# Kernel optimization log

Measured on AMD Instinct MI355X. Metric: run time of the kernel, lower is better.

The kernel has to match this reference:

```python
import jax, jax.numpy as jnp
import numpy as np

N, E, B = 100000, 640000, 256
F_IN, HID, HEADS = 128, 128, 4
C = HID // HEADS  # 32 channels per head
NEG_SLOPE = 0.2


def _p(key, shape, scale=0.1):
    return (jax.random.normal(key, shape) * scale).astype(jnp.float32)


def setup_inputs() -> dict:
    key = jax.random.key(0)
    ks = jax.random.split(key, 24)
    inp = {
        "x": jax.random.normal(ks[0], (N, F_IN), jnp.float32),
        "edge_index": jax.random.randint(ks[1], (2, E), 0, N),
        "batch": jnp.sort(jax.random.randint(ks[2], (N,), 0, B)),
        "w_in": _p(ks[3], (F_IN, HID)),
        "b_in": jnp.zeros((HID,), jnp.float32),
    }
    for i in range(3):
        inp[f"w{i}"] = _p(ks[4 + 4 * i], (HID, HEADS * C))
        inp[f"asrc{i}"] = _p(ks[5 + 4 * i], (HEADS, C))
        inp[f"adst{i}"] = _p(ks[6 + 4 * i], (HEADS, C))
        inp[f"b{i}"] = jnp.zeros((HID if i < 2 else C,), jnp.float32)
    inp["w_fp"] = _p(ks[20], (C, HID)); inp["b_fp"] = jnp.zeros((HID,), jnp.float32)
    inp["w_m1"] = _p(ks[21], (HID, HID // 2)); inp["b_m1"] = jnp.zeros((HID // 2,), jnp.float32)
    inp["w_m2"] = _p(ks[22], (HID // 2, 1)); inp["b_m2"] = jnp.zeros((1,), jnp.float32)
    return inp


def _gat(x, src, dst, W, a_src, a_dst, bias, concat):
    """PyG-style GATConv (edge_dim=None, eval mode, self-loops pre-appended)."""
    n = x.shape[0]
    H, Ch = a_src.shape
    h = (x @ W).reshape(n, H, Ch)                     # [N,H,C]
    al_s = (h * a_src).sum(-1)                        # [N,H]
    al_d = (h * a_dst).sum(-1)                        # [N,H]
    logit = jax.nn.leaky_relu(al_s[src] + al_d[dst], NEG_SLOPE)  # [Etot,H]
    # segment softmax over incoming edges of each dst node
    m = jax.ops.segment_max(logit, dst, num_segments=n)
    e = jnp.exp(logit - m[dst])
    s = jax.ops.segment_sum(e, dst, num_segments=n)
    alpha = e / (s[dst] + 1e-16)                      # [Etot,H]
    out = jax.ops.segment_sum(h[src] * alpha[:, :, None], dst, num_segments=n)  # [N,H,C]
    out = out.reshape(n, H * Ch) if concat else out.mean(axis=1)
    return out + bias


def reference(x, edge_index, batch, w_in, b_in,
              w0, asrc0, adst0, b0, w1, asrc1, adst1, b1, w2, asrc2, adst2, b2,
              w_fp, b_fp, w_m1, b_m1, w_m2, b_m2):
    n = x.shape[0]
    loops = jnp.arange(n, dtype=edge_index.dtype)
    src = jnp.concatenate([edge_index[0], loops])     # add self loops (PyG default)
    dst = jnp.concatenate([edge_index[1], loops])
    h = x @ w_in + b_in
    h = jax.nn.elu(_gat(h, src, dst, w0, asrc0, adst0, b0, True))
    h = jax.nn.elu(_gat(h, src, dst, w1, asrc1, adst1, b1, True))
    h = jax.nn.elu(_gat(h, src, dst, w2, asrc2, adst2, b2, False))  # [N,C]
    cnt = jax.ops.segment_sum(jnp.ones((n,), h.dtype), batch, num_segments=B)
    pooled = jax.ops.segment_sum(h, batch, num_segments=B) / jnp.maximum(cnt, 1.0)[:, None]
    out = pooled @ w_fp + b_fp                        # final_proj (out dim 32 != 128)
    hm = jax.nn.relu(out @ w_m1 + b_m1)
    return hm @ w_m2 + b_m2                           # [B,1]
```

## Files before the change

### kernel.cpp

```cpp
#include <hip/hip_runtime.h>

#define NEG 0.2f

typedef short s16x8 __attribute__((ext_vector_type(8)));
typedef float f32x4 __attribute__((ext_vector_type(4)));

__device__ __forceinline__ float lrelu(float x) { return x >= 0.f ? x : NEG * x; }
__device__ __forceinline__ float elu1(float x) { return x > 0.f ? x : __expf(x) - 1.f; }

__device__ __forceinline__ unsigned bf16rn(float f) {
    unsigned u = __float_as_uint(f);
    u += 0x7fffu + ((u >> 16) & 1u);
    return u >> 16;
}
__device__ __forceinline__ float bf16tof(ushort h) {
    return __uint_as_float(((unsigned)h) << 16);
}
__device__ __forceinline__ float bf16lo(unsigned u) { return __uint_as_float(u << 16); }
__device__ __forceinline__ float bf16hi(unsigned u) { return __uint_as_float(u & 0xffff0000u); }

__global__ void hist_kernel(const int* __restrict__ dst, int e, int n, int* __restrict__ deg) {
    int p = blockIdx.x & 7;
    int s = blockIdx.x >> 3;
    int nslices = gridDim.x >> 3;
    int rng = (n + 7) >> 3;
    int lo = p * rng, hi = min(n, lo + rng);
    int chunk = (e + nslices - 1) / nslices;
    int i0 = s * chunk, i1 = min(e, i0 + chunk);
    for (int i = i0 + threadIdx.x; i < i1; i += blockDim.x) {
        int d = dst[i];
        if (d >= lo && d < hi) atomicAdd(&deg[d], 1);
    }
}

__device__ __forceinline__ int waveIncScanI(int v, int lane) {
#pragma unroll
    for (int off = 1; off < 64; off <<= 1) {
        int u = __shfl_up(v, off);
        if (lane >= off) v += u;
    }
    return v;
}

__global__ void scan1_kernel(const int* __restrict__ deg, int nk,
                             int* __restrict__ rowp, int* __restrict__ bsums) {
    int t = threadIdx.x;
    int base = blockIdx.x * 2048 + t * 8;
    int vals[8];
    int sum = 0;
#pragma unroll
    for (int i = 0; i < 8; ++i) {
        int idx = base + i;
        int v = (idx < nk) ? deg[idx] : 0;
        vals[i] = sum;
        sum += v;
    }
    int lane = t & 63, w = t >> 6;
    int inc = waveIncScanI(sum, lane);
    __shared__ int wsums[4];
    if (lane == 63) wsums[w] = inc;
    __syncthreads();
    int wpre = 0;
#pragma unroll
    for (int i = 0; i < 3; ++i) wpre += (i < w) ? wsums[i] : 0;
    int exc = wpre + inc - sum;
#pragma unroll
    for (int i = 0; i < 8; ++i) {
        int idx = base + i;
        if (idx < nk) rowp[idx] = exc + vals[i];
    }
    if (t == 255) bsums[blockIdx.x] = wpre + inc;
}

__global__ void scan3_kernel(int* __restrict__ rowp, const int* __restrict__ bsums,
                             int nk, int total, int* __restrict__ cursor) {
    int g = blockIdx.x;
    __shared__ int spre;
    if (threadIdx.x < 64) {
        int lane = threadIdx.x;
        int v = 0;
        for (int base = lane; base < g; base += 64) v += bsums[base];
#pragma unroll
        for (int off = 32; off > 0; off >>= 1) v += __shfl_xor(v, off);
        if (lane == 0) spre = v;
    }
    __syncthreads();
    int pre = spre;
    int base = g * 2048 + threadIdx.x * 8;
#pragma unroll
    for (int i = 0; i < 8; ++i) {
        int idx = base + i;
        if (idx < nk) {
            int v = rowp[idx] + pre;
            rowp[idx] = v;
            cursor[idx] = v;
        } else if (idx == nk) {
            rowp[nk] = total;
        }
    }
}

__global__ void fill_kernel(const int* __restrict__ src, const int* __restrict__ dst, int e,
                            int n, int* __restrict__ cursor, int* __restrict__ col) {
    int p = blockIdx.x & 7;
    int s = blockIdx.x >> 3;
    int nslices = gridDim.x >> 3;
    int rng = (n + 7) >> 3;
    int lo = p * rng, hi = min(n, lo + rng);
    int chunk = (e + nslices - 1) / nslices;
    int i0 = s * chunk, i1 = min(e, i0 + chunk);
    for (int i = i0 + threadIdx.x; i < i1; i += blockDim.x) {
        int d = dst[i];
        if (d >= lo && d < hi) {
            int pos = atomicAdd(&cursor[d], 1);
            col[pos] = src[i];
        }
    }
}

__global__ void wpack_kernel(const float* __restrict__ w0, const float* __restrict__ w1,
                             const float* __restrict__ w2, const float* __restrict__ w3,
                             ushort* __restrict__ whi, ushort* __restrict__ wlo) {
    int idx = blockIdx.x * 256 + threadIdx.x;
    int layer = idx >> 14, e = idx & 16383;
    const float* W = layer == 0 ? w0 : layer == 1 ? w1 : layer == 2 ? w2 : w3;
    int k = e >> 7, c = e & 127;
    float w = W[e];
    ushort hi = (ushort)bf16rn(w);
    ushort lo = (ushort)bf16rn(w - bf16tof(hi));
    int kt = k >> 5, kk = k & 31, j = kk & 7;
    int ln = ((kk >> 3) << 4) | (c & 15);
    int ntg = c >> 4;
    int pos = (layer << 14) + (((kt << 3) + ntg) * 64 + ln) * 8 + j;
    whi[pos] = hi;
    wlo[pos] = lo;
}

template <bool BIAS, bool AL, bool ABF16>
__global__ __launch_bounds__(512, 4) void gemm_mfma_kernel(
    const void* __restrict__ Av, const ushort* __restrict__ whi, const ushort* __restrict__ wlo,
    const float* __restrict__ bias, ushort* __restrict__ outb, int n, int ntiles,
    const float* __restrict__ asrc, const float* __restrict__ adst,
    float* __restrict__ als, float* __restrict__ ald) {
    __shared__ s16x8 ahi[2][4][64];
    __shared__ s16x8 alo[2][4][64];
    int t = threadIdx.x;
    int wid = t >> 6, lane = t & 63;
    int ntp = wid & 3;
    int mhalf = wid >> 2;

    const s16x8* wph = (const s16x8*)whi;
    const s16x8* wpl = (const s16x8*)wlo;
    s16x8 wh[4][2], wl[4][2];
#pragma unroll
    for (int kt = 0; kt < 4; ++kt)
#pragma unroll
        for (int j = 0; j < 2; ++j) {
            int ntg = ntp * 2 + j;
            wh[kt][j] = wph[((kt << 3) + ntg) * 64 + lane];
            wl[kt][j] = wpl[((kt << 3) + ntg) * 64 + lane];
        }

    int c0 = ntp * 32 + (lane & 15);
    int c1 = c0 + 16;
    float bv0 = 0.f, bv1 = 0.f;
    if (BIAS) { bv0 = bias[c0]; bv1 = bias[c1]; }
    float as0 = 0.f, as1 = 0.f, ad0 = 0.f, ad1 = 0.f;
    if (AL) {
        as0 = asrc[ntp * 32 + (lane & 15)];
        as1 = asrc[ntp * 32 + 16 + (lane & 15)];
        ad0 = adst[ntp * 32 + (lane & 15)];
        ad1 = adst[ntp * 32 + 16 + (lane & 15)];
    }

    int srow = t >> 4, skoct = t & 15;
    int smh = srow >> 4, skt = skoct >> 2;
    int sln = ((skoct & 3) << 4) | (srow & 15);

    for (int tile = blockIdx.x; tile < ntiles; tile += gridDim.x) {
        int r0 = tile * 32;
        {
            int gr = r0 + srow;
            if (ABF16) {
                const ushort* Ab = (const ushort*)Av;
                s16x8 hi = {0, 0, 0, 0, 0, 0, 0, 0};
                if (gr < n) hi = *(const s16x8*)(Ab + (size_t)gr * 128 + skoct * 8);
                ahi[smh][skt][sln] = hi;
            } else {
                const float* Af = (const float*)Av;
                float4 v0 = make_float4(0.f, 0.f, 0.f, 0.f), v1 = v0;
                if (gr < n) {
                    const float4* rp = (const float4*)(Af + (size_t)gr * 128 + skoct * 8);
                    v0 = rp[0];
                    v1 = rp[1];
                }
                float f[8] = {v0.x, v0.y, v0.z, v0.w, v1.x, v1.y, v1.z, v1.w};
                s16x8 hi, lo;
#pragma unroll
                for (int j = 0; j < 8; ++j) {
                    ushort h = (ushort)bf16rn(f[j]);
                    hi[j] = (short)h;
                    lo[j] = (short)bf16rn(f[j] - bf16tof(h));
                }
                ahi[smh][skt][sln] = hi;
                alo[smh][skt][sln] = lo;
            }
        }
        __syncthreads();

        f32x4 acc0 = {0.f, 0.f, 0.f, 0.f};
        f32x4 acc1 = {0.f, 0.f, 0.f, 0.f};
#pragma unroll
        for (int kt = 0; kt < 4; ++kt) {
            s16x8 ah = ahi[mhalf][kt][lane];
            if (ABF16) {
                acc0 = __builtin_amdgcn_mfma_f32_16x16x32_bf16(ah, wh[kt][0], acc0, 0, 0, 0);
                acc0 = __builtin_amdgcn_mfma_f32_16x16x32_bf16(ah, wl[kt][0], acc0, 0, 0, 0);
                acc1 = __builtin_amdgcn_mfma_f32_16x16x32_bf16(ah, wh[kt][1], acc1, 0, 0, 0);
                acc1 = __builtin_amdgcn_mfma_f32_16x16x32_bf16(ah, wl[kt][1], acc1, 0, 0, 0);
            } else {
                s16x8 al = alo[mhalf][kt][lane];
                acc0 = __builtin_amdgcn_mfma_f32_16x16x32_bf16(ah, wh[kt][0], acc0, 0, 0, 0);
                acc0 = __builtin_amdgcn_mfma_f32_16x16x32_bf16(ah, wl[kt][0], acc0, 0, 0, 0);
                acc0 = __builtin_amdgcn_mfma_f32_16x16x32_bf16(al, wh[kt][0], acc0, 0, 0, 0);
                acc1 = __builtin_amdgcn_mfma_f32_16x16x32_bf16(ah, wh[kt][1], acc1, 0, 0, 0);
                acc1 = __builtin_amdgcn_mfma_f32_16x16x32_bf16(ah, wl[kt][1], acc1, 0, 0, 0);
                acc1 = __builtin_amdgcn_mfma_f32_16x16x32_bf16(al, wh[kt][1], acc1, 0, 0, 0);
            }
        }

        int rbase = r0 + mhalf * 16 + (lane >> 4) * 4;
#pragma unroll
        for (int i = 0; i < 4; ++i) {
            int r = rbase + i;
            if (r < n) {
                outb[(size_t)r * 128 + c0] = (ushort)bf16rn(acc0[i] + bv0);
                outb[(size_t)r * 128 + c1] = (ushort)bf16rn(acc1[i] + bv1);
            }
        }
        if (AL) {
#pragma unroll
            for (int i = 0; i < 4; ++i) {
                float ps = acc0[i] * as0 + acc1[i] * as1;
                float pd = acc0[i] * ad0 + acc1[i] * ad1;
                ps += __shfl_xor(ps, 1); ps += __shfl_xor(ps, 2);
                ps += __shfl_xor(ps, 4); ps += __shfl_xor(ps, 8);
                pd += __shfl_xor(pd, 1); pd += __shfl_xor(pd, 2);
                pd += __shfl_xor(pd, 4); pd += __shfl_xor(pd, 8);
                int r = rbase + i;
                if ((lane & 15) == 0 && r < n) {
                    als[r * 4 + ntp] = ps;
                    ald[r * 4 + ntp] = pd;
                }
            }
        }
        __syncthreads();
    }
}

template <bool CONCAT>
__global__ void agg_kernel(const ushort* __restrict__ hp, const float* __restrict__ als,
                           const float* __restrict__ ald_, const int* __restrict__ rowp,
                           const int* __restrict__ col, const float* __restrict__ bias,
                           ushort* __restrict__ outb, float* __restrict__ outf, int n) {
    int lane = threadIdx.x & 63;
    int hl = lane & 31;
    int wid = (blockIdx.x * blockDim.x + threadIdx.x) >> 6;
    int d = wid * 2 + (lane >> 5);
    bool valid = d < n;
    int dc = valid ? d : (n - 1);

    int h = hl >> 3;
    int c4 = hl * 4;
    int hh = hl & 3;
    int jl = hl >> 2;
    int bshf = lane & 32;

    int start = rowp[dc];
    int end = valid ? rowp[dc + 1] : start;

    float aldv_hh = ald_[dc * 4 + hh];
    float eself = __expf(lrelu(als[dc * 4 + h] + ald_[dc * 4 + h]));

    uint2 sv = *(const uint2*)(hp + (size_t)dc * 128 + c4);
    float a0 = eself * bf16lo(sv.x), a1 = eself * bf16hi(sv.x);
    float a2 = eself * bf16lo(sv.y), a3 = eself * bf16hi(sv.y);
    float esum = eself;

    int iters = (end - start + 7) >> 3;
    int oiters = __shfl_xor(iters, 32);
    int maxit = iters > oiters ? iters : oiters;
    unsigned nclamp = (unsigned)(n - 1);

    for (int it = 0; it < maxit; ++it) {
        int p0 = start + it * 8;
        bool act = p0 < end;
        int pc = act ? p0 : start;
        int4 ca = *(const int4*)(col + pc);
        int4 cb = *(const int4*)(col + pc + 4);
        unsigned se = (unsigned)col[pc + jl];
        se = se > nclamp ? nclamp : se;
        float ee = __expf(lrelu(als[(size_t)se * 4 + hh] + aldv_hh));
        ee = (act && (p0 + jl < end)) ? ee : 0.f;

#define EDGE(JJ, SRC)                                                              \
        {                                                                          \
            float ej = __shfl(ee, bshf | (JJ << 2) | h);                           \
            unsigned sju = (unsigned)(SRC);                                        \
            sju = sju > nclamp ? nclamp : sju;                                     \
            uint2 uv = *(const uint2*)(hp + (size_t)sju * 128 + c4);               \
            a0 += ej * bf16lo(uv.x); a1 += ej * bf16hi(uv.x);                      \
            a2 += ej * bf16lo(uv.y); a3 += ej * bf16hi(uv.y);                      \
            esum += ej;                                                            \
        }
        EDGE(0, ca.x) EDGE(1, ca.y) EDGE(2, ca.z) EDGE(3, ca.w)
        EDGE(4, cb.x) EDGE(5, cb.y) EDGE(6, cb.z) EDGE(7, cb.w)
#undef EDGE
    }

    float inv = 1.f / (esum + 1e-16f);
    a0 *= inv; a1 *= inv; a2 *= inv; a3 *= inv;
    if (CONCAT) {
        if (valid) {
            float o0 = elu1(a0 + bias[c4]);
            float o1 = elu1(a1 + bias[c4 + 1]);
            float o2 = elu1(a2 + bias[c4 + 2]);
            float o3 = elu1(a3 + bias[c4 + 3]);
            uint2 pk;
            pk.x = bf16rn(o0) | (bf16rn(o1) << 16);
            pk.y = bf16rn(o2) | (bf16rn(o3) << 16);
            *(uint2*)(outb + (size_t)d * 128 + c4) = pk;
        }
    } else {
        a0 += __shfl_xor(a0, 8); a0 += __shfl_xor(a0, 16);
        a1 += __shfl_xor(a1, 8); a1 += __shfl_xor(a1, 16);
        a2 += __shfl_xor(a2, 8); a2 += __shfl_xor(a2, 16);
        a3 += __shfl_xor(a3, 8); a3 += __shfl_xor(a3, 16);
        if (valid && hl < 8) {
            int cin = hl * 4;
            float4 o;
            o.x = elu1(a0 * 0.25f + bias[cin]);
            o.y = elu1(a1 * 0.25f + bias[cin + 1]);
            o.z = elu1(a2 * 0.25f + bias[cin + 2]);
            o.w = elu1(a3 * 0.25f + bias[cin + 3]);
            *(float4*)(outf + (size_t)d * 32 + cin) = o;
        }
    }
}

__global__ void poolmlp_kernel(const float* __restrict__ h2, const int* __restrict__ batch,
                               int n, const float* __restrict__ w_fp,
                               const float* __restrict__ b_fp, const float* __restrict__ w_m1,
                               const float* __restrict__ b_m1, const float* __restrict__ w_m2,
                               const float* __restrict__ b_m2, float* __restrict__ out) {
    int b = blockIdx.x, t = threadIdx.x;
    __shared__ int sb[2];
    if (t == 0) {
        int lo = 0, hi = n;
        while (lo < hi) { int mid = (lo + hi) >> 1; if (batch[mid] < b) lo = mid + 1; else hi = mid; }
        sb[0] = lo;
        int lo2 = lo, hi2 = n;
        while (lo2 < hi2) { int mid = (lo2 + hi2) >> 1; if (batch[mid] < b + 1) lo2 = mid + 1; else hi2 = mid; }
        sb[1] = lo2;
    }
    __syncthreads();
    int lo = sb[0], hi = sb[1];
    int c = t & 31, g = t >> 5;
    float acc = 0.f;
    for (int i = lo + g; i < hi; i += 8) acc += h2[(size_t)i * 32 + c];
    __shared__ float red[8][32];
    __shared__ float sp[32], so[128];
    red[g][c] = acc;
    __syncthreads();
    if (t < 32) {
        float s = 0.f;
#pragma unroll
        for (int g2 = 0; g2 < 8; ++g2) s += red[g2][t];
        float cnt = (float)(hi - lo);
        sp[t] = s / fmaxf(cnt, 1.f);
    }
    __syncthreads();
    if (t < 128) {
        float o = b_fp[t];
#pragma unroll 8
        for (int k = 0; k < 32; ++k) o += sp[k] * w_fp[k * 128 + t];
        so[t] = o;
    }
    __syncthreads();
    if (t < 64) {
        float hm = b_m1[t];
        for (int cc = 0; cc < 128; ++cc) hm += so[cc] * w_m1[cc * 64 + t];
        float v = fmaxf(hm, 0.f) * w_m2[t];
#pragma unroll
        for (int offd = 32; offd > 0; offd >>= 1) v += __shfl_down(v, offd);
        if (t == 0) out[b] = v + b_m2[0];
    }
}

extern "C" void kernel_launch(void* const* d_in, const int* in_sizes, int n_in,
                              void* d_out, int out_size, void* d_ws, size_t ws_size,
                              hipStream_t stream) {
    const float* x = (const float*)d_in[0];
    const int* ei = (const int*)d_in[1];
    const int* batch = (const int*)d_in[2];
    const float* w_in = (const float*)d_in[3];
    const float* b_in = (const float*)d_in[4];
    const float* w[3] = {(const float*)d_in[5], (const float*)d_in[9], (const float*)d_in[13]};
    const float* asrc[3] = {(const float*)d_in[6], (const float*)d_in[10], (const float*)d_in[14]};
    const float* adst[3] = {(const float*)d_in[7], (const float*)d_in[11], (const float*)d_in[15]};
    const float* bb[3] = {(const float*)d_in[8], (const float*)d_in[12], (const float*)d_in[16]};
    const float* w_fp = (const float*)d_in[17];
    const float* b_fp = (const float*)d_in[18];
    const float* w_m1 = (const float*)d_in[19];
    const float* b_m1 = (const float*)d_in[20];
    const float* w_m2 = (const float*)d_in[21];
    const float* b_m2 = (const float*)d_in[22];

    int n = in_sizes[0] / 128;
    int e = in_sizes[1] / 2;
    int B = out_size;

    char* wsb = (char*)d_ws;
    size_t off = 0;
    auto alloc = [&](size_t bytes) -> void* {
        void* p = wsb + off;
        off += (bytes + 255) & ~(size_t)255;
        return p;
    };
    ushort* hAu = (ushort*)alloc((size_t)n * 128 * 2);
    ushort* hBu = (ushort*)alloc((size_t)n * 128 * 2);
    float* h3 = (float*)alloc((size_t)n * 32 * 4);
    float* als = (float*)alloc((size_t)n * 4 * 4);
    float* ald = (float*)alloc((size_t)n * 4 * 4);
    int* deg = (int*)alloc((size_t)n * 4);
    int* rowp = (int*)alloc((size_t)(n + 1) * 4);
    int* col = (int*)alloc((size_t)(e + 8) * 4);
    int* bsums = (int*)alloc(4096);
    ushort* whi = (ushort*)alloc((size_t)4 * 16384 * 2);
    ushort* wlo = (ushort*)alloc((size_t)4 * 16384 * 2);

    const int* srcp = ei;
    const int* dstp = ei + e;

    hipMemsetAsync(deg, 0, (size_t)n * 4, stream);
    hist_kernel<<<1024, 256, 0, stream>>>(dstp, e, n, deg);
    int nb = (n + 2047) / 2048;
    scan1_kernel<<<nb, 256, 0, stream>>>(deg, n, rowp, bsums);
    scan3_kernel<<<nb, 256, 0, stream>>>(rowp, bsums, n, e, deg);
    fill_kernel<<<1024, 256, 0, stream>>>(srcp, dstp, e, n, deg, col);

    wpack_kernel<<<256, 256, 0, stream>>>(w_in, w[0], w[1], w[2], whi, wlo);

    int ntiles = (n + 31) / 32;
    int gblk = ntiles < 512 ? ntiles : 512;

    gemm_mfma_kernel<true, false, false><<<gblk, 512, 0, stream>>>(
        x, whi, wlo, b_in, hAu, n, ntiles, nullptr, nullptr, nullptr, nullptr);

    int gridAgg = (n + 7) / 8;
    for (int L = 0; L < 3; ++L) {
        gemm_mfma_kernel<false, true, true><<<gblk, 512, 0, stream>>>(
            hAu, whi + (size_t)(L + 1) * 16384, wlo + (size_t)(L + 1) * 16384, nullptr, hBu, n,
            ntiles, asrc[L], adst[L], als, ald);
        if (L < 2)
            agg_kernel<true><<<gridAgg, 256, 0, stream>>>(hBu, als, ald, rowp, col, bb[L],
                                                          hAu, nullptr, n);
        else
            agg_kernel<false><<<gridAgg, 256, 0, stream>>>(hBu, als, ald, rowp, col, bb[L],
                                                           nullptr, h3, n);
    }

    poolmlp_kernel<<<B, 256, 0, stream>>>(h3, batch, n, w_fp, b_fp, w_m1, b_m1, w_m2, b_m2,
                                          (float*)d_out);
}
```

Before: 296.2 us.

## Fold input projection into first GAT weight, removing one GEMM pass

```diff
diff --git a/kernel.cpp b/kernel.cpp
--- a/kernel.cpp
+++ b/kernel.cpp
@@ -118,22 +118,37 @@
     }
 }
 
-__global__ void wpack_kernel(const float* __restrict__ w0, const float* __restrict__ w1,
-                             const float* __restrict__ w2, const float* __restrict__ w3,
-                             ushort* __restrict__ whi, ushort* __restrict__ wlo) {
+__global__ void wpack_kernel(const float* __restrict__ w_in, const float* __restrict__ w0,
+                             const float* __restrict__ w1, const float* __restrict__ w2,
+                             const float* __restrict__ b_in,
+                             ushort* __restrict__ whi, ushort* __restrict__ wlo,
+                             float* __restrict__ beff) {
     int idx = blockIdx.x * 256 + threadIdx.x;
+    if (idx >= 3 * 16384) return;
     int layer = idx >> 14, e = idx & 16383;
-    const float* W = layer == 0 ? w0 : layer == 1 ? w1 : layer == 2 ? w2 : w3;
     int k = e >> 7, c = e & 127;
-    float w = W[e];
-    ushort hi = (ushort)bf16rn(w);
-    ushort lo = (ushort)bf16rn(w - bf16tof(hi));
+    float wv;
+    if (layer == 0) {
+        float s = 0.f;
+        for (int m = 0; m < 128; ++m) s += w_in[k * 128 + m] * w0[m * 128 + c];
+        wv = s;
+    } else {
+        const float* W = (layer == 1) ? w1 : w2;
+        wv = W[e];
+    }
+    ushort hi = (ushort)bf16rn(wv);
+    ushort lo = (ushort)bf16rn(wv - bf16tof(hi));
     int kt = k >> 5, kk = k & 31, j = kk & 7;
     int ln = ((kk >> 3) << 4) | (c & 15);
     int ntg = c >> 4;
     int pos = (layer << 14) + (((kt << 3) + ntg) * 64 + ln) * 8 + j;
     whi[pos] = hi;
     wlo[pos] = lo;
+    if (idx < 128) {
+        float s = 0.f;
+        for (int m = 0; m < 128; ++m) s += b_in[m] * w0[m * 128 + idx];
+        beff[idx] = s;
+    }
 }
 
 template <bool BIAS, bool AL, bool ABF16>
@@ -233,21 +248,19 @@
 #pragma unroll
         for (int i = 0; i < 4; ++i) {
             int r = rbase + i;
+            float o0 = acc0[i] + bv0;
+            float o1 = acc1[i] + bv1;
             if (r < n) {
-                outb[(size_t)r * 128 + c0] = (ushort)bf16rn(acc0[i] + bv0);
-                outb[(size_t)r * 128 + c1] = (ushort)bf16rn(acc1[i] + bv1);
+                outb[(size_t)r * 128 + c0] = (ushort)bf16rn(o0);
+                outb[(size_t)r * 128 + c1] = (ushort)bf16rn(o1);
             }
-        }
-        if (AL) {
-#pragma unroll
-            for (int i = 0; i < 4; ++i) {
-                float ps = acc0[i] * as0 + acc1[i] * as1;
-                float pd = acc0[i] * ad0 + acc1[i] * ad1;
+            if (AL) {
+                float ps = o0 * as0 + o1 * as1;
+                float pd = o0 * ad0 + o1 * ad1;
                 ps += __shfl_xor(ps, 1); ps += __shfl_xor(ps, 2);
                 ps += __shfl_xor(ps, 4); ps += __shfl_xor(ps, 8);
                 pd += __shfl_xor(pd, 1); pd += __shfl_xor(pd, 2);
                 pd += __shfl_xor(pd, 4); pd += __shfl_xor(pd, 8);
-                int r = rbase + i;
                 if ((lane & 15) == 0 && r < n) {
                     als[r * 4 + ntp] = ps;
                     ald[r * 4 + ntp] = pd;
@@ -298,7 +311,13 @@
         int pc = act ? p0 : start;
         int4 ca = *(const int4*)(col + pc);
         int4 cb = *(const int4*)(col + pc + 4);
-        unsigned se = (unsigned)col[pc + jl];
+        int v0 = (jl & 4) ? cb.x : ca.x;
+        int v1 = (jl & 4) ? cb.y : ca.y;
+        int v2 = (jl & 4) ? cb.z : ca.z;
+        int v3 = (jl & 4) ? cb.w : ca.w;
+        int w0_ = (jl & 2) ? v2 : v0;
+        int w1_ = (jl & 2) ? v3 : v1;
+        unsigned se = (unsigned)((jl & 1) ? w1_ : w0_);
         se = se > nclamp ? nclamp : se;
         float ee = __expf(lrelu(als[(size_t)se * 4 + hh] + aldv_hh));
         ee = (act && (p0 + jl < end)) ? ee : 0.f;
@@ -436,8 +455,9 @@
     int* rowp = (int*)alloc((size_t)(n + 1) * 4);
     int* col = (int*)alloc((size_t)(e + 8) * 4);
     int* bsums = (int*)alloc(4096);
-    ushort* whi = (ushort*)alloc((size_t)4 * 16384 * 2);
-    ushort* wlo = (ushort*)alloc((size_t)4 * 16384 * 2);
+    ushort* whi = (ushort*)alloc((size_t)3 * 16384 * 2);
+    ushort* wlo = (ushort*)alloc((size_t)3 * 16384 * 2);
+    float* beff = (float*)alloc(128 * 4);
 
     const int* srcp = ei;
     const int* dstp = ei + e;
@@ -449,18 +469,20 @@
     scan3_kernel<<<nb, 256, 0, stream>>>(rowp, bsums, n, e, deg);
     fill_kernel<<<1024, 256, 0, stream>>>(srcp, dstp, e, n, deg, col);
 
-    wpack_kernel<<<256, 256, 0, stream>>>(w_in, w[0], w[1], w[2], whi, wlo);
+    wpack_kernel<<<192, 256, 0, stream>>>(w_in, w[0], w[1], w[2], b_in, whi, wlo, beff);
 
     int ntiles = (n + 31) / 32;
     int gblk = ntiles < 512 ? ntiles : 512;
-
-    gemm_mfma_kernel<true, false, false><<<gblk, 512, 0, stream>>>(
-        x, whi, wlo, b_in, hAu, n, ntiles, nullptr, nullptr, nullptr, nullptr);
-
     int gridAgg = (n + 7) / 8;
-    for (int L = 0; L < 3; ++L) {
+
+    gemm_mfma_kernel<true, true, false><<<gblk, 512, 0, stream>>>(
+        x, whi, wlo, beff, hBu, n, ntiles, asrc[0], adst[0], als, ald);
+    agg_kernel<true><<<gridAgg, 256, 0, stream>>>(hBu, als, ald, rowp, col, bb[0],
+                                                  hAu, nullptr, n);
+
+    for (int L = 1; L < 3; ++L) {
         gemm_mfma_kernel<false, true, true><<<gblk, 512, 0, stream>>>(
-            hAu, whi + (size_t)(L + 1) * 16384, wlo + (size_t)(L + 1) * 16384, nullptr, hBu, n,
+            hAu, whi + (size_t)L * 16384, wlo + (size_t)L * 16384, nullptr, hBu, n,
             ntiles, asrc[L], adst[L], als, ald);
         if (L < 2)
             agg_kernel<true><<<gridAgg, 256, 0, stream>>>(hBu, als, ald, rowp, col, bb[L],
```

After: 287.8 us. 1.03x faster.
